# Kernel optimization log

Measured on AMD Instinct MI355X. Metric: run time of the kernel, lower is better.

Reference implementation:

```python
import jax, jax.numpy as jnp
import numpy as np

B = 2048
D = 256
C = 100000
SCALE = 30.0
MARGIN = 0.2
EPS = 1e-6


def setup_inputs() -> dict:
    key = jax.random.key(0)
    k1, k2, k3 = jax.random.split(key, 3)
    emb = jax.random.normal(k1, (B, D), dtype=jnp.float32)
    # speaker embeddings are typically L2-normalized; also keeps cosines in (-1,1)
    emb = emb / jnp.linalg.norm(emb, axis=1, keepdims=True)
    W = jax.random.normal(k2, (C, D), dtype=jnp.float32)
    targets = jax.random.randint(k3, (B,), 0, C, dtype=jnp.int64)
    return {"embedding": emb, "W": W, "targets": targets}


def reference(embedding, W, targets):
    # normalize classifier rows (F.normalize on weight, dim=1, eps=1e-12)
    Wn = W / jnp.maximum(jnp.linalg.norm(W, axis=1, keepdims=True), 1e-12)
    # [B, C] cosine logits, clamped as in the original
    cos = jnp.clip(embedding @ Wn.T, -1.0, 1.0)
    # per-sample target cosine -> margin-adjusted numerator
    tgt_cos = jnp.take_along_axis(cos, targets[:, None], axis=1)[:, 0]
    numerator = SCALE * jnp.cos(jnp.arccos(tgt_cos) + MARGIN)  # [B]
    # masked sum over non-target classes (replaces the python loop + cat)
    col = jnp.arange(C, dtype=targets.dtype)[None, :]
    not_target = (col != targets[:, None]).astype(cos.dtype)  # [B, C]
    excl_sum = jnp.sum(jnp.exp(SCALE * cos) * not_target, axis=1)  # [B]
    denominator = jnp.exp(numerator) + excl_sum
    loss = -jnp.mean(numerator - jnp.log(denominator + EPS))
    return loss
```

## Files before the change

### kernel.cpp

```cpp
#include <hip/hip_runtime.h>
#include <hip/hip_bf16.h>


static constexpr int Bn = 2048;
static constexpr int Dn = 256;
static constexpr int Cn = 100000;
static constexpr int NCBLK  = 782;
static constexpr int CPAD   = NCBLK * 128;
static constexpr int SLICES = NCBLK * 4;
static constexpr float OOB_COLS = (float)(CPAD - Cn);
static constexpr int NTILE = Bn / 32;

#define SCALE_F 30.0f
#define MARGIN_F 0.2f
#define EPS_F 1e-6f

typedef __attribute__((ext_vector_type(8))) short bf16x8;
typedef __attribute__((ext_vector_type(4))) float f32x4;
typedef __attribute__((address_space(3))) unsigned int lds_u32;
typedef const __attribute__((address_space(1))) unsigned int g_u32;

__device__ __forceinline__ void async_cp16(const void* g, void* lds) {
    __builtin_amdgcn_global_load_lds((g_u32*)g, (lds_u32*)lds, 16, 0, 0);
}

__device__ __forceinline__ short f2bf_rne(float x) {
    union { float f; unsigned int u; } v; v.f = x;
    unsigned int r = v.u + 0x7fffu + ((v.u >> 16) & 1u);
    return (short)(r >> 16);
}

__global__ __launch_bounds__(256) void k_emb2bf(const float* __restrict__ emb,
                                                short* __restrict__ out) {
    int i = (blockIdx.x * 256 + threadIdx.x) * 4;
    float4 x = *(const float4*)(emb + i);
    short4 o;
    o.x = f2bf_rne(x.x); o.y = f2bf_rne(x.y);
    o.z = f2bf_rne(x.z); o.w = f2bf_rne(x.w);
    *(short4*)(out + i) = o;
}

__global__ __launch_bounds__(256) void k_wnorm(const float* __restrict__ W,
                                               short* __restrict__ Wn) {
    const int r    = blockIdx.x * 4 + (threadIdx.x >> 6);
    const int lane = threadIdx.x & 63;
    float4 x = {0.f, 0.f, 0.f, 0.f};
    if (r < Cn) x = *(const float4*)(W + (size_t)r * Dn + lane * 4);
    float ss = x.x * x.x + x.y * x.y + x.z * x.z + x.w * x.w;
#pragma unroll
    for (int o = 1; o < 64; o <<= 1) ss += __shfl_xor(ss, o);
    const float rn = 1.0f / fmaxf(sqrtf(ss), 1e-12f);
    short4 o;
    o.x = f2bf_rne(x.x * rn); o.y = f2bf_rne(x.y * rn);
    o.z = f2bf_rne(x.z * rn); o.w = f2bf_rne(x.w * rn);
    *(short4*)(Wn + (size_t)r * Dn + lane * 4) = o;
}

template <bool USE_WN>
__global__ __launch_bounds__(256, 3) void k_main(const float* __restrict__ W,
                                                 const short* __restrict__ Wn,
                                                 const short* __restrict__ embbf,
                                                 float* __restrict__ partial) {
    __shared__ __align__(16) short stage[2 * 32 * 256];

    const int tid  = threadIdx.x;
    const int wave = tid >> 6;
    const int lane = tid & 63;
    const int q    = lane >> 4;
    const int cr   = lane & 15;
    const int sw   = cr & 7;

    const int cblk  = blockIdx.x;
    const int cbase = cblk * 128 + wave * 32;

    auto stage_tile = [&](int t, int buf) {
        short* dst = stage + buf * (32 * 256);
#pragma unroll
        for (int i = 0; i < 4; ++i) {
            const int r0 = wave * 8 + 2 * i;
            const int rl = r0 + (lane >> 5);
            const int c16 = (lane & 31) ^ (rl & 7);
            const short* g = embbf + (size_t)(t * 32 + rl) * Dn + c16 * 8;
            async_cp16(g, dst + r0 * 256);
        }
    };

    stage_tile(0, 0);

    bf16x8 afrag[2][8];
    if (USE_WN) {
#pragma unroll
        for (int ct = 0; ct < 2; ++ct) {
            const short* wr = Wn + (size_t)(cbase + ct * 16 + cr) * Dn + q * 8;
#pragma unroll
            for (int ks = 0; ks < 8; ++ks)
                afrag[ct][ks] = *(const bf16x8*)(wr + ks * 32);
        }
    } else {
#pragma unroll
        for (int ct = 0; ct < 2; ++ct) {
            const int c = cbase + ct * 16 + cr;
            const float* wr = W + (size_t)c * Dn;
            float ss = 0.0f;
            if (c < Cn) {
#pragma unroll
                for (int ks = 0; ks < 8; ++ks) {
                    float4 x0 = *(const float4*)(wr + ks * 32 + q * 8);
                    float4 x1 = *(const float4*)(wr + ks * 32 + q * 8 + 4);
                    ss += x0.x * x0.x + x0.y * x0.y + x0.z * x0.z + x0.w * x0.w;
                    ss += x1.x * x1.x + x1.y * x1.y + x1.z * x1.z + x1.w * x1.w;
                }
            }
            ss += __shfl_xor(ss, 16);
            ss += __shfl_xor(ss, 32);
            const float rn = 1.0f / fmaxf(sqrtf(ss), 1e-12f);
#pragma unroll
            for (int ks = 0; ks < 8; ++ks) {
                bf16x8 a = {0, 0, 0, 0, 0, 0, 0, 0};
                if (c < Cn) {
                    float4 x0 = *(const float4*)(wr + ks * 32 + q * 8);
                    float4 x1 = *(const float4*)(wr + ks * 32 + q * 8 + 4);
                    a[0] = f2bf_rne(x0.x * rn); a[1] = f2bf_rne(x0.y * rn);
                    a[2] = f2bf_rne(x0.z * rn); a[3] = f2bf_rne(x0.w * rn);
                    a[4] = f2bf_rne(x1.x * rn); a[5] = f2bf_rne(x1.y * rn);
                    a[6] = f2bf_rne(x1.z * rn); a[7] = f2bf_rne(x1.w * rn);
                }
                afrag[ct][ks] = a;
            }
        }
    }

    __syncthreads();

    float* pout = partial + (size_t)(cblk * 4 + wave) * Bn;

    for (int it = 0; it < NTILE; ++it) {
        const int buf = it & 1;
        if (it + 1 < NTILE) stage_tile(it + 1, buf ^ 1);

        const short* sb = stage + buf * (32 * 256);
#pragma unroll
        for (int st = 0; st < 2; ++st) {
            const short* rowp = sb + (st * 16 + cr) * 256;
            bf16x8 bfrag[8];
#pragma unroll
            for (int ks = 0; ks < 8; ++ks)
                bfrag[ks] = *(const bf16x8*)(rowp + ((((ks << 2) | q) ^ sw) << 3));

            f32x4 acc0 = {0.f, 0.f, 0.f, 0.f};
            f32x4 acc1 = {0.f, 0.f, 0.f, 0.f};
#pragma unroll
            for (int ks = 0; ks < 8; ++ks) {
                acc0 = __builtin_amdgcn_mfma_f32_16x16x32_bf16(afrag[0][ks], bfrag[ks], acc0, 0, 0, 0);
                acc1 = __builtin_amdgcn_mfma_f32_16x16x32_bf16(afrag[1][ks], bfrag[ks], acc1, 0, 0, 0);
            }

            float s = 0.0f;
#pragma unroll
            for (int r = 0; r < 4; ++r) {
                s += __expf(SCALE_F * fminf(fmaxf(acc0[r], -1.f), 1.f));
                s += __expf(SCALE_F * fminf(fmaxf(acc1[r], -1.f), 1.f));
            }
            s += __shfl_xor(s, 16);
            s += __shfl_xor(s, 32);
            if (lane < 16) pout[it * 32 + st * 16 + cr] = s;
        }
        __syncthreads();
    }
}

__global__ __launch_bounds__(256) void k_target(const float* __restrict__ emb,
                                                const float* __restrict__ W,
                                                const int* __restrict__ tgt,
                                                float* __restrict__ numv,
                                                float* __restrict__ etv) {
    const int b    = blockIdx.x * 4 + (threadIdx.x >> 6);
    const int lane = threadIdx.x & 63;
    const int t    = tgt[b];
    float4 x = *(const float4*)(W + (size_t)t * Dn + lane * 4);
    float4 e = *(const float4*)(emb + b * Dn + lane * 4);
    float dot = x.x * e.x + x.y * e.y + x.z * e.z + x.w * e.w;
    float ss  = x.x * x.x + x.y * x.y + x.z * x.z + x.w * x.w;
#pragma unroll
    for (int o = 1; o < 64; o <<= 1) {
        dot += __shfl_xor(dot, o);
        ss  += __shfl_xor(ss, o);
    }
    if (lane == 0) {
        float cosv = dot / fmaxf(sqrtf(ss), 1e-12f);
        cosv = fminf(fmaxf(cosv, -1.f), 1.f);
        const float num = SCALE_F * cosf(acosf(cosv) + MARGIN_F);
        numv[b] = num;
        etv[b]  = __expf(SCALE_F * cosv);
    }
}

static constexpr int SCHUNK = 98;
__global__ __launch_bounds__(256) void k_rowsum(const float* __restrict__ partial,
                                                float* __restrict__ rowsum) {
    const int b  = blockIdx.x * 256 + threadIdx.x;
    const int s0 = blockIdx.y * SCHUNK;
    const int s1 = min(s0 + SCHUNK, SLICES);
    float acc = 0.0f;
    for (int s = s0; s < s1; ++s) acc += partial[(size_t)s * Bn + b];
    atomicAdd(&rowsum[b], acc);
}

__global__ __launch_bounds__(256) void k_loss(const float* __restrict__ numv,
                                              const float* __restrict__ etv,
                                              const float* __restrict__ rowsum,
                                              float* __restrict__ out) {
    float acc = 0.0f;
    for (int b = threadIdx.x; b < Bn; b += 256) {
        const float num  = numv[b];
        const float excl = rowsum[b] - OOB_COLS - etv[b];
        const float denom = __expf(num) + excl;
        acc += num - logf(denom + EPS_F);
    }
#pragma unroll
    for (int o = 1; o < 64; o <<= 1) acc += __shfl_xor(acc, o);
    __shared__ float sa[4];
    const int wave = threadIdx.x >> 6, lane = threadIdx.x & 63;
    if (lane == 0) sa[wave] = acc;
    __syncthreads();
    if (threadIdx.x == 0) out[0] = -(sa[0] + sa[1] + sa[2] + sa[3]) / (float)Bn;
}

extern "C" void kernel_launch(void* const* d_in, const int* in_sizes, int n_in,
                              void* d_out, int out_size, void* d_ws, size_t ws_size,
                              hipStream_t stream) {
    const float* emb = (const float*)d_in[0];
    const float* W   = (const float*)d_in[1];
    const int*   tgt = (const int*)d_in[2];
    float* out = (float*)d_out;

    char* ws = (char*)d_ws;
    short* embbf   = (short*)ws;
    float* partial = (float*)(ws + (1 << 20));
    float* rowsum  = partial + (size_t)SLICES * Bn;
    float* numv    = rowsum + Bn;
    float* etv     = numv + Bn;
    short* Wnorm   = (short*)(etv + Bn);

    const size_t need_full = (size_t)((char*)Wnorm - ws) + (size_t)CPAD * Dn * sizeof(short);
    const bool use_wn = ws_size >= need_full;

    hipMemsetAsync(rowsum, 0, Bn * sizeof(float), stream);
    k_emb2bf<<<512, 256, 0, stream>>>(emb, embbf);
    if (use_wn) {
        k_wnorm<<<CPAD / 4, 256, 0, stream>>>(W, Wnorm);
        k_main<true><<<NCBLK, 256, 0, stream>>>(W, Wnorm, embbf, partial);
    } else {
        k_main<false><<<NCBLK, 256, 0, stream>>>(W, Wnorm, embbf, partial);
    }
    k_target<<<Bn / 4, 256, 0, stream>>>(emb, W, tgt, numv, etv);
    k_rowsum<<<dim3(Bn / 256, 32), 256, 0, stream>>>(partial, rowsum);
    k_loss<<<1, 256, 0, stream>>>(numv, etv, rowsum, out);
}
```

Baseline: 318.7 us.

## Merge prep kernels, accumulate row sums in LDS, and fuse reduction with loss

Puts the weight normalization, embedding bf16 conversion and target-cosine computation into one prep kernel. The main kernel now accumulates per-row exp sums across its four waves with LDS atomics, so it writes one partial row per block instead of four. A single finish kernel then reduces the partials and computes the loss, replacing the separate rowsum and loss kernels. The change also raises the occupancy hint to 4, splits the B-fragment loads into two halves to cut register pressure, and drops the cosine clamp in the exp path. That clamp removal can change numerics slightly for values above 1 after bf16 rounding.

```diff
diff --git a/kernel.cpp b/kernel.cpp
--- a/kernel.cpp
+++ b/kernel.cpp
@@ -7,7 +7,6 @@
 static constexpr int Cn = 100000;
 static constexpr int NCBLK  = 782;
 static constexpr int CPAD   = NCBLK * 128;
-static constexpr int SLICES = NCBLK * 4;
 static constexpr float OOB_COLS = (float)(CPAD - Cn);
 static constexpr int NTILE = Bn / 32;
 
@@ -30,38 +29,69 @@
     return (short)(r >> 16);
 }
 
-__global__ __launch_bounds__(256) void k_emb2bf(const float* __restrict__ emb,
-                                                short* __restrict__ out) {
-    int i = (blockIdx.x * 256 + threadIdx.x) * 4;
-    float4 x = *(const float4*)(emb + i);
-    short4 o;
-    o.x = f2bf_rne(x.x); o.y = f2bf_rne(x.y);
-    o.z = f2bf_rne(x.z); o.w = f2bf_rne(x.w);
-    *(short4*)(out + i) = o;
-}
-
-__global__ __launch_bounds__(256) void k_wnorm(const float* __restrict__ W,
-                                               short* __restrict__ Wn) {
-    const int r    = blockIdx.x * 4 + (threadIdx.x >> 6);
-    const int lane = threadIdx.x & 63;
-    float4 x = {0.f, 0.f, 0.f, 0.f};
-    if (r < Cn) x = *(const float4*)(W + (size_t)r * Dn + lane * 4);
-    float ss = x.x * x.x + x.y * x.y + x.z * x.z + x.w * x.w;
-#pragma unroll
-    for (int o = 1; o < 64; o <<= 1) ss += __shfl_xor(ss, o);
-    const float rn = 1.0f / fmaxf(sqrtf(ss), 1e-12f);
-    short4 o;
-    o.x = f2bf_rne(x.x * rn); o.y = f2bf_rne(x.y * rn);
-    o.z = f2bf_rne(x.z * rn); o.w = f2bf_rne(x.w * rn);
-    *(short4*)(Wn + (size_t)r * Dn + lane * 4) = o;
+static constexpr int PB_WN  = CPAD / 4;
+static constexpr int PB_EMB = PB_WN + 512;
+static constexpr int PB_TGT = PB_EMB + 512;
+__global__ __launch_bounds__(256) void k_prep(const float* __restrict__ W,
+                                              const float* __restrict__ emb,
+                                              const int* __restrict__ tgt,
+                                              short* __restrict__ Wn,
+                                              short* __restrict__ embbf,
+                                              float* __restrict__ numv,
+                                              float* __restrict__ etv,
+                                              int write_wn) {
+    const int blk = blockIdx.x;
+    if (blk < PB_WN) {
+        if (!write_wn) return;
+        const int r    = blk * 4 + (threadIdx.x >> 6);
+        const int lane = threadIdx.x & 63;
+        float4 x = {0.f, 0.f, 0.f, 0.f};
+        if (r < Cn) x = *(const float4*)(W + (size_t)r * Dn + lane * 4);
+        float ss = x.x * x.x + x.y * x.y + x.z * x.z + x.w * x.w;
+#pragma unroll
+        for (int o = 1; o < 64; o <<= 1) ss += __shfl_xor(ss, o);
+        const float rn = 1.0f / fmaxf(sqrtf(ss), 1e-12f);
+        short4 o;
+        o.x = f2bf_rne(x.x * rn); o.y = f2bf_rne(x.y * rn);
+        o.z = f2bf_rne(x.z * rn); o.w = f2bf_rne(x.w * rn);
+        *(short4*)(Wn + (size_t)r * Dn + lane * 4) = o;
+    } else if (blk < PB_EMB) {
+        const int i = ((blk - PB_WN) * 256 + threadIdx.x) * 4;
+        float4 x = *(const float4*)(emb + i);
+        short4 o;
+        o.x = f2bf_rne(x.x); o.y = f2bf_rne(x.y);
+        o.z = f2bf_rne(x.z); o.w = f2bf_rne(x.w);
+        *(short4*)(embbf + i) = o;
+    } else {
+        const int b    = (blk - PB_EMB) * 4 + (threadIdx.x >> 6);
+        const int lane = threadIdx.x & 63;
+        const int t    = tgt[b];
+        float4 x = *(const float4*)(W + (size_t)t * Dn + lane * 4);
+        float4 e = *(const float4*)(emb + b * Dn + lane * 4);
+        float dot = x.x * e.x + x.y * e.y + x.z * e.z + x.w * e.w;
+        float ss  = x.x * x.x + x.y * x.y + x.z * x.z + x.w * x.w;
+#pragma unroll
+        for (int o = 1; o < 64; o <<= 1) {
+            dot += __shfl_xor(dot, o);
+            ss  += __shfl_xor(ss, o);
+        }
+        if (lane == 0) {
+            float cosv = dot / fmaxf(sqrtf(ss), 1e-12f);
+            cosv = fminf(fmaxf(cosv, -1.f), 1.f);
+            const float num = SCALE_F * cosf(acosf(cosv) + MARGIN_F);
+            numv[b] = num;
+            etv[b]  = __expf(SCALE_F * cosv);
+        }
+    }
 }
 
 template <bool USE_WN>
-__global__ __launch_bounds__(256, 3) void k_main(const float* __restrict__ W,
+__global__ __launch_bounds__(256, 4) void k_main(const float* __restrict__ W,
                                                  const short* __restrict__ Wn,
                                                  const short* __restrict__ embbf,
                                                  float* __restrict__ partial) {
     __shared__ __align__(16) short stage[2 * 32 * 256];
+    __shared__ float rowAcc[Bn];
 
     const int tid  = threadIdx.x;
     const int wave = tid >> 6;
@@ -86,6 +116,8 @@
     };
 
     stage_tile(0, 0);
+
+    for (int i = tid; i < Bn; i += 256) rowAcc[i] = 0.0f;
 
     bf16x8 afrag[2][8];
     if (USE_WN) {
@@ -132,8 +164,6 @@
 
     __syncthreads();
 
-    float* pout = partial + (size_t)(cblk * 4 + wave) * Bn;
-
     for (int it = 0; it < NTILE; ++it) {
         const int buf = it & 1;
         if (it + 1 < NTILE) stage_tile(it + 1, buf ^ 1);
@@ -142,88 +172,69 @@
 #pragma unroll
         for (int st = 0; st < 2; ++st) {
             const short* rowp = sb + (st * 16 + cr) * 256;
-            bf16x8 bfrag[8];
-#pragma unroll
-            for (int ks = 0; ks < 8; ++ks)
-                bfrag[ks] = *(const bf16x8*)(rowp + ((((ks << 2) | q) ^ sw) << 3));
-
             f32x4 acc0 = {0.f, 0.f, 0.f, 0.f};
             f32x4 acc1 = {0.f, 0.f, 0.f, 0.f};
 #pragma unroll
-            for (int ks = 0; ks < 8; ++ks) {
-                acc0 = __builtin_amdgcn_mfma_f32_16x16x32_bf16(afrag[0][ks], bfrag[ks], acc0, 0, 0, 0);
-                acc1 = __builtin_amdgcn_mfma_f32_16x16x32_bf16(afrag[1][ks], bfrag[ks], acc1, 0, 0, 0);
+            for (int half = 0; half < 2; ++half) {
+                bf16x8 bf[4];
+#pragma unroll
+                for (int j = 0; j < 4; ++j) {
+                    const int ks = half * 4 + j;
+                    bf[j] = *(const bf16x8*)(rowp + ((((ks << 2) | q) ^ sw) << 3));
+                }
+#pragma unroll
+                for (int j = 0; j < 4; ++j) {
+                    const int ks = half * 4 + j;
+                    acc0 = __builtin_amdgcn_mfma_f32_16x16x32_bf16(afrag[0][ks], bf[j], acc0, 0, 0, 0);
+                    acc1 = __builtin_amdgcn_mfma_f32_16x16x32_bf16(afrag[1][ks], bf[j], acc1, 0, 0, 0);
+                }
             }
 
             float s = 0.0f;
 #pragma unroll
             for (int r = 0; r < 4; ++r) {
-                s += __expf(SCALE_F * fminf(fmaxf(acc0[r], -1.f), 1.f));
-                s += __expf(SCALE_F * fminf(fmaxf(acc1[r], -1.f), 1.f));
+                s += __expf(SCALE_F * acc0[r]);
+                s += __expf(SCALE_F * acc1[r]);
             }
             s += __shfl_xor(s, 16);
             s += __shfl_xor(s, 32);
-            if (lane < 16) pout[it * 32 + st * 16 + cr] = s;
+            if (lane < 16) atomicAdd(&rowAcc[it * 32 + st * 16 + cr], s);
         }
         __syncthreads();
     }
-}
-
-__global__ __launch_bounds__(256) void k_target(const float* __restrict__ emb,
-                                                const float* __restrict__ W,
-                                                const int* __restrict__ tgt,
-                                                float* __restrict__ numv,
-                                                float* __restrict__ etv) {
-    const int b    = blockIdx.x * 4 + (threadIdx.x >> 6);
-    const int lane = threadIdx.x & 63;
-    const int t    = tgt[b];
-    float4 x = *(const float4*)(W + (size_t)t * Dn + lane * 4);
-    float4 e = *(const float4*)(emb + b * Dn + lane * 4);
-    float dot = x.x * e.x + x.y * e.y + x.z * e.z + x.w * e.w;
-    float ss  = x.x * x.x + x.y * x.y + x.z * x.z + x.w * x.w;
-#pragma unroll
-    for (int o = 1; o < 64; o <<= 1) {
-        dot += __shfl_xor(dot, o);
-        ss  += __shfl_xor(ss, o);
-    }
-    if (lane == 0) {
-        float cosv = dot / fmaxf(sqrtf(ss), 1e-12f);
-        cosv = fminf(fmaxf(cosv, -1.f), 1.f);
-        const float num = SCALE_F * cosf(acosf(cosv) + MARGIN_F);
-        numv[b] = num;
-        etv[b]  = __expf(SCALE_F * cosv);
-    }
-}
-
-static constexpr int SCHUNK = 98;
-__global__ __launch_bounds__(256) void k_rowsum(const float* __restrict__ partial,
-                                                float* __restrict__ rowsum) {
-    const int b  = blockIdx.x * 256 + threadIdx.x;
-    const int s0 = blockIdx.y * SCHUNK;
-    const int s1 = min(s0 + SCHUNK, SLICES);
+
+    float* pout = partial + (size_t)cblk * Bn;
+    for (int i = tid; i < Bn; i += 256) pout[i] = rowAcc[i];
+}
+
+__global__ __launch_bounds__(256) void k_finish(const float* __restrict__ partial,
+                                                const float* __restrict__ numv,
+                                                const float* __restrict__ etv,
+                                                float* __restrict__ out) {
+    __shared__ float red[64];
+    const int l  = threadIdx.x & 63;
+    const int qq = threadIdx.x >> 6;
+    const int b  = blockIdx.x * 64 + l;
+
+    if (threadIdx.x < 64) red[threadIdx.x] = 0.0f;
+    __syncthreads();
+
+    const int s0 = qq * 196;
+    const int s1 = min(s0 + 196, NCBLK);
     float acc = 0.0f;
     for (int s = s0; s < s1; ++s) acc += partial[(size_t)s * Bn + b];
-    atomicAdd(&rowsum[b], acc);
-}
-
-__global__ __launch_bounds__(256) void k_loss(const float* __restrict__ numv,
-                                              const float* __restrict__ etv,
-                                              const float* __restrict__ rowsum,
-                                              float* __restrict__ out) {
-    float acc = 0.0f;
-    for (int b = threadIdx.x; b < Bn; b += 256) {
+    atomicAdd(&red[l], acc);
+    __syncthreads();
+
+    if (threadIdx.x < 64) {
         const float num  = numv[b];
-        const float excl = rowsum[b] - OOB_COLS - etv[b];
+        const float excl = red[l] - OOB_COLS - etv[b];
         const float denom = __expf(num) + excl;
-        acc += num - logf(denom + EPS_F);
-    }
-#pragma unroll
-    for (int o = 1; o < 64; o <<= 1) acc += __shfl_xor(acc, o);
-    __shared__ float sa[4];
-    const int wave = threadIdx.x >> 6, lane = threadIdx.x & 63;
-    if (lane == 0) sa[wave] = acc;
-    __syncthreads();
-    if (threadIdx.x == 0) out[0] = -(sa[0] + sa[1] + sa[2] + sa[3]) / (float)Bn;
+        float term = num - logf(denom + EPS_F);
+#pragma unroll
+        for (int o = 1; o < 64; o <<= 1) term += __shfl_xor(term, o);
+        if (l == 0) atomicAdd(out, -term / (float)Bn);
+    }
 }
 
 extern "C" void kernel_launch(void* const* d_in, const int* in_sizes, int n_in,
@@ -237,23 +248,19 @@
     char* ws = (char*)d_ws;
     short* embbf   = (short*)ws;
     float* partial = (float*)(ws + (1 << 20));
-    float* rowsum  = partial + (size_t)SLICES * Bn;
-    float* numv    = rowsum + Bn;
+    float* numv    = partial + (size_t)NCBLK * Bn;
     float* etv     = numv + Bn;
     short* Wnorm   = (short*)(etv + Bn);
 
     const size_t need_full = (size_t)((char*)Wnorm - ws) + (size_t)CPAD * Dn * sizeof(short);
     const bool use_wn = ws_size >= need_full;
 
-    hipMemsetAsync(rowsum, 0, Bn * sizeof(float), stream);
-    k_emb2bf<<<512, 256, 0, stream>>>(emb, embbf);
+    hipMemsetAsync(out, 0, sizeof(float), stream);
+    k_prep<<<PB_TGT, 256, 0, stream>>>(W, emb, tgt, Wnorm, embbf, numv, etv, use_wn ? 1 : 0);
     if (use_wn) {
-        k_wnorm<<<CPAD / 4, 256, 0, stream>>>(W, Wnorm);
         k_main<true><<<NCBLK, 256, 0, stream>>>(W, Wnorm, embbf, partial);
     } else {
         k_main<false><<<NCBLK, 256, 0, stream>>>(W, Wnorm, embbf, partial);
     }
-    k_target<<<Bn / 4, 256, 0, stream>>>(emb, W, tgt, numv, etv);
-    k_rowsum<<<dim3(Bn / 256, 32), 256, 0, stream>>>(partial, rowsum);
-    k_loss<<<1, 256, 0, stream>>>(numv, etv, rowsum, out);
-}
+    k_finish<<<Bn / 64, 256, 0, stream>>>(partial, numv, etv, out);
+}
```

New measurement: 359.8 us. 12.9% more time.

## Fuse prep kernels, normalize W inside main kernel, raise occupancy

Applied to the files above, without the earlier changes.

Merges the embedding bf16 conversion and the target-cosine computation into a single prep launch. Drops the separate W-normalization pass and its bf16 workspace, so the main kernel always normalizes W rows itself. Raises the occupancy hint to 4 blocks per CU, loads B fragments in two halves to reduce register pressure, and removes the clamp before exp. The aim is fewer launches and less global traffic from the Wn write and re-read, at the cost of doing the fp32 W loads and normalization inside the GEMM kernel.

```diff
diff --git a/kernel.cpp b/kernel.cpp
--- a/kernel.cpp
+++ b/kernel.cpp
@@ -30,35 +30,44 @@
     return (short)(r >> 16);
 }
 
-__global__ __launch_bounds__(256) void k_emb2bf(const float* __restrict__ emb,
-                                                short* __restrict__ out) {
-    int i = (blockIdx.x * 256 + threadIdx.x) * 4;
-    float4 x = *(const float4*)(emb + i);
-    short4 o;
-    o.x = f2bf_rne(x.x); o.y = f2bf_rne(x.y);
-    o.z = f2bf_rne(x.z); o.w = f2bf_rne(x.w);
-    *(short4*)(out + i) = o;
-}
-
-__global__ __launch_bounds__(256) void k_wnorm(const float* __restrict__ W,
-                                               short* __restrict__ Wn) {
-    const int r    = blockIdx.x * 4 + (threadIdx.x >> 6);
-    const int lane = threadIdx.x & 63;
-    float4 x = {0.f, 0.f, 0.f, 0.f};
-    if (r < Cn) x = *(const float4*)(W + (size_t)r * Dn + lane * 4);
-    float ss = x.x * x.x + x.y * x.y + x.z * x.z + x.w * x.w;
-#pragma unroll
-    for (int o = 1; o < 64; o <<= 1) ss += __shfl_xor(ss, o);
-    const float rn = 1.0f / fmaxf(sqrtf(ss), 1e-12f);
-    short4 o;
-    o.x = f2bf_rne(x.x * rn); o.y = f2bf_rne(x.y * rn);
-    o.z = f2bf_rne(x.z * rn); o.w = f2bf_rne(x.w * rn);
-    *(short4*)(Wn + (size_t)r * Dn + lane * 4) = o;
-}
-
-template <bool USE_WN>
-__global__ __launch_bounds__(256, 3) void k_main(const float* __restrict__ W,
-                                                 const short* __restrict__ Wn,
+__global__ __launch_bounds__(256) void k_prep(const float* __restrict__ W,
+                                              const float* __restrict__ emb,
+                                              const int* __restrict__ tgt,
+                                              short* __restrict__ embbf,
+                                              float* __restrict__ numv,
+                                              float* __restrict__ etv) {
+    const int blk = blockIdx.x;
+    if (blk < 512) {
+        const int i = (blk * 256 + threadIdx.x) * 4;
+        float4 x = *(const float4*)(emb + i);
+        short4 o;
+        o.x = f2bf_rne(x.x); o.y = f2bf_rne(x.y);
+        o.z = f2bf_rne(x.z); o.w = f2bf_rne(x.w);
+        *(short4*)(embbf + i) = o;
+    } else {
+        const int b    = (blk - 512) * 4 + (threadIdx.x >> 6);
+        const int lane = threadIdx.x & 63;
+        const int t    = tgt[b];
+        float4 x = *(const float4*)(W + (size_t)t * Dn + lane * 4);
+        float4 e = *(const float4*)(emb + b * Dn + lane * 4);
+        float dot = x.x * e.x + x.y * e.y + x.z * e.z + x.w * e.w;
+        float ss  = x.x * x.x + x.y * x.y + x.z * x.z + x.w * x.w;
+#pragma unroll
+        for (int o = 1; o < 64; o <<= 1) {
+            dot += __shfl_xor(dot, o);
+            ss  += __shfl_xor(ss, o);
+        }
+        if (lane == 0) {
+            float cosv = dot / fmaxf(sqrtf(ss), 1e-12f);
+            cosv = fminf(fmaxf(cosv, -1.f), 1.f);
+            const float num = SCALE_F * cosf(acosf(cosv) + MARGIN_F);
+            numv[b] = num;
+            etv[b]  = __expf(SCALE_F * cosv);
+        }
+    }
+}
+
+__global__ __launch_bounds__(256, 4) void k_main(const float* __restrict__ W,
                                                  const short* __restrict__ embbf,
                                                  float* __restrict__ partial) {
     __shared__ __align__(16) short stage[2 * 32 * 256];
@@ -88,45 +97,35 @@
     stage_tile(0, 0);
 
     bf16x8 afrag[2][8];
-    if (USE_WN) {
-#pragma unroll
-        for (int ct = 0; ct < 2; ++ct) {
-            const short* wr = Wn + (size_t)(cbase + ct * 16 + cr) * Dn + q * 8;
-#pragma unroll
-            for (int ks = 0; ks < 8; ++ks)
-                afrag[ct][ks] = *(const bf16x8*)(wr + ks * 32);
-        }
-    } else {
-#pragma unroll
-        for (int ct = 0; ct < 2; ++ct) {
-            const int c = cbase + ct * 16 + cr;
-            const float* wr = W + (size_t)c * Dn;
-            float ss = 0.0f;
+#pragma unroll
+    for (int ct = 0; ct < 2; ++ct) {
+        const int c = cbase + ct * 16 + cr;
+        const float* wr = W + (size_t)c * Dn;
+        float ss = 0.0f;
+        if (c < Cn) {
+#pragma unroll
+            for (int ks = 0; ks < 8; ++ks) {
+                float4 x0 = *(const float4*)(wr + ks * 32 + q * 8);
+                float4 x1 = *(const float4*)(wr + ks * 32 + q * 8 + 4);
+                ss += x0.x * x0.x + x0.y * x0.y + x0.z * x0.z + x0.w * x0.w;
+                ss += x1.x * x1.x + x1.y * x1.y + x1.z * x1.z + x1.w * x1.w;
+            }
+        }
+        ss += __shfl_xor(ss, 16);
+        ss += __shfl_xor(ss, 32);
+        const float rn = 1.0f / fmaxf(sqrtf(ss), 1e-12f);
+#pragma unroll
+        for (int ks = 0; ks < 8; ++ks) {
+            bf16x8 a = {0, 0, 0, 0, 0, 0, 0, 0};
             if (c < Cn) {
-#pragma unroll
-                for (int ks = 0; ks < 8; ++ks) {
-                    float4 x0 = *(const float4*)(wr + ks * 32 + q * 8);
-                    float4 x1 = *(const float4*)(wr + ks * 32 + q * 8 + 4);
-                    ss += x0.x * x0.x + x0.y * x0.y + x0.z * x0.z + x0.w * x0.w;
-                    ss += x1.x * x1.x + x1.y * x1.y + x1.z * x1.z + x1.w * x1.w;
-                }
-            }
-            ss += __shfl_xor(ss, 16);
-            ss += __shfl_xor(ss, 32);
-            const float rn = 1.0f / fmaxf(sqrtf(ss), 1e-12f);
-#pragma unroll
-            for (int ks = 0; ks < 8; ++ks) {
-                bf16x8 a = {0, 0, 0, 0, 0, 0, 0, 0};
-                if (c < Cn) {
-                    float4 x0 = *(const float4*)(wr + ks * 32 + q * 8);
-                    float4 x1 = *(const float4*)(wr + ks * 32 + q * 8 + 4);
-                    a[0] = f2bf_rne(x0.x * rn); a[1] = f2bf_rne(x0.y * rn);
-                    a[2] = f2bf_rne(x0.z * rn); a[3] = f2bf_rne(x0.w * rn);
-                    a[4] = f2bf_rne(x1.x * rn); a[5] = f2bf_rne(x1.y * rn);
-                    a[6] = f2bf_rne(x1.z * rn); a[7] = f2bf_rne(x1.w * rn);
-                }
-                afrag[ct][ks] = a;
-            }
+                float4 x0 = *(const float4*)(wr + ks * 32 + q * 8);
+                float4 x1 = *(const float4*)(wr + ks * 32 + q * 8 + 4);
+                a[0] = f2bf_rne(x0.x * rn); a[1] = f2bf_rne(x0.y * rn);
+                a[2] = f2bf_rne(x0.z * rn); a[3] = f2bf_rne(x0.w * rn);
+                a[4] = f2bf_rne(x1.x * rn); a[5] = f2bf_rne(x1.y * rn);
+                a[6] = f2bf_rne(x1.z * rn); a[7] = f2bf_rne(x1.w * rn);
+            }
+            afrag[ct][ks] = a;
         }
     }
 
@@ -142,56 +141,35 @@
 #pragma unroll
         for (int st = 0; st < 2; ++st) {
             const short* rowp = sb + (st * 16 + cr) * 256;
-            bf16x8 bfrag[8];
-#pragma unroll
-            for (int ks = 0; ks < 8; ++ks)
-                bfrag[ks] = *(const bf16x8*)(rowp + ((((ks << 2) | q) ^ sw) << 3));
-
             f32x4 acc0 = {0.f, 0.f, 0.f, 0.f};
             f32x4 acc1 = {0.f, 0.f, 0.f, 0.f};
 #pragma unroll
-            for (int ks = 0; ks < 8; ++ks) {
-                acc0 = __builtin_amdgcn_mfma_f32_16x16x32_bf16(afrag[0][ks], bfrag[ks], acc0, 0, 0, 0);
-                acc1 = __builtin_amdgcn_mfma_f32_16x16x32_bf16(afrag[1][ks], bfrag[ks], acc1, 0, 0, 0);
+            for (int half = 0; half < 2; ++half) {
+                bf16x8 bf[4];
+#pragma unroll
+                for (int j = 0; j < 4; ++j) {
+                    const int ks = half * 4 + j;
+                    bf[j] = *(const bf16x8*)(rowp + ((((ks << 2) | q) ^ sw) << 3));
+                }
+#pragma unroll
+                for (int j = 0; j < 4; ++j) {
+                    const int ks = half * 4 + j;
+                    acc0 = __builtin_amdgcn_mfma_f32_16x16x32_bf16(afrag[0][ks], bf[j], acc0, 0, 0, 0);
+                    acc1 = __builtin_amdgcn_mfma_f32_16x16x32_bf16(afrag[1][ks], bf[j], acc1, 0, 0, 0);
+                }
             }
 
             float s = 0.0f;
 #pragma unroll
             for (int r = 0; r < 4; ++r) {
-                s += __expf(SCALE_F * fminf(fmaxf(acc0[r], -1.f), 1.f));
-                s += __expf(SCALE_F * fminf(fmaxf(acc1[r], -1.f), 1.f));
+                s += __expf(SCALE_F * acc0[r]);
+                s += __expf(SCALE_F * acc1[r]);
             }
             s += __shfl_xor(s, 16);
             s += __shfl_xor(s, 32);
             if (lane < 16) pout[it * 32 + st * 16 + cr] = s;
         }
         __syncthreads();
-    }
-}
-
-__global__ __launch_bounds__(256) void k_target(const float* __restrict__ emb,
-                                                const float* __restrict__ W,
-                                                const int* __restrict__ tgt,
-                                                float* __restrict__ numv,
-                                                float* __restrict__ etv) {
-    const int b    = blockIdx.x * 4 + (threadIdx.x >> 6);
-    const int lane = threadIdx.x & 63;
-    const int t    = tgt[b];
-    float4 x = *(const float4*)(W + (size_t)t * Dn + lane * 4);
-    float4 e = *(const float4*)(emb + b * Dn + lane * 4);
-    float dot = x.x * e.x + x.y * e.y + x.z * e.z + x.w * e.w;
-    float ss  = x.x * x.x + x.y * x.y + x.z * x.z + x.w * x.w;
-#pragma unroll
-    for (int o = 1; o < 64; o <<= 1) {
-        dot += __shfl_xor(dot, o);
-        ss  += __shfl_xor(ss, o);
-    }
-    if (lane == 0) {
-        float cosv = dot / fmaxf(sqrtf(ss), 1e-12f);
-        cosv = fminf(fmaxf(cosv, -1.f), 1.f);
-        const float num = SCALE_F * cosf(acosf(cosv) + MARGIN_F);
-        numv[b] = num;
-        etv[b]  = __expf(SCALE_F * cosv);
     }
 }
 
@@ -240,20 +218,10 @@
     float* rowsum  = partial + (size_t)SLICES * Bn;
     float* numv    = rowsum + Bn;
     float* etv     = numv + Bn;
-    short* Wnorm   = (short*)(etv + Bn);
-
-    const size_t need_full = (size_t)((char*)Wnorm - ws) + (size_t)CPAD * Dn * sizeof(short);
-    const bool use_wn = ws_size >= need_full;
 
     hipMemsetAsync(rowsum, 0, Bn * sizeof(float), stream);
-    k_emb2bf<<<512, 256, 0, stream>>>(emb, embbf);
-    if (use_wn) {
-        k_wnorm<<<CPAD / 4, 256, 0, stream>>>(W, Wnorm);
-        k_main<true><<<NCBLK, 256, 0, stream>>>(W, Wnorm, embbf, partial);
-    } else {
-        k_main<false><<<NCBLK, 256, 0, stream>>>(W, Wnorm, embbf, partial);
-    }
-    k_target<<<Bn / 4, 256, 0, stream>>>(emb, W, tgt, numv, etv);
+    k_prep<<<1024, 256, 0, stream>>>(W, emb, tgt, embbf, numv, etv);
+    k_main<<<NCBLK, 256, 0, stream>>>(W, embbf, partial);
     k_rowsum<<<dim3(Bn / 256, 32), 256, 0, stream>>>(partial, rowsum);
     k_loss<<<1, 256, 0, stream>>>(numv, etv, rowsum, out);
 }
```

Measured after the change: 309.2 us. 3.0% less time.
